# Kernel optimization log

Hardware: AMD Instinct MI355X
Metric: run time of the kernel (lower is better)

Reference implementation:

```python
import jax, jax.numpy as jnp
import numpy as np

B = 4096
INPUT = 1024
HIDDEN = 2048
D_INNER = 2 * HIDDEN      # expand=2
DT_RANK = HIDDEN // 16    # 128
D_STATE = 16
LN_EPS = 1e-5


def setup_inputs() -> dict:
    key = jax.random.key(0)
    ks = jax.random.split(key, 12)
    s = lambda fan_in: 1.0 / np.sqrt(fan_in)
    inp = {
        "x": jax.random.normal(ks[0], (B, INPUT), jnp.float32),
        "h": jax.random.normal(ks[1], (B, HIDDEN), jnp.float32),
        # in_proj: Linear(input_size, 2*d_inner, bias=False)
        "W_in": jax.random.uniform(ks[2], (2 * D_INNER, INPUT), jnp.float32, -s(INPUT), s(INPUT)),
        # state_proj: Linear(hidden, d_inner, bias=False)
        "W_state": jax.random.uniform(ks[3], (D_INNER, HIDDEN), jnp.float32, -s(HIDDEN), s(HIDDEN)),
        # x_proj: Linear(d_inner, dt_rank + 2*d_state, bias=False)
        "W_xproj": jax.random.uniform(ks[4], (DT_RANK + 2 * D_STATE, D_INNER), jnp.float32, -s(D_INNER), s(D_INNER)),
        # dt_proj: Linear(dt_rank, d_inner, bias=True), weight ~ U(-dt_rank^-0.5, dt_rank^-0.5)
        "W_dt": jax.random.uniform(ks[5], (D_INNER, DT_RANK), jnp.float32, -s(DT_RANK), s(DT_RANK)),
        "b_dt": jnp.log(jnp.expm1(jnp.exp(jax.random.uniform(ks[6], (D_INNER,), jnp.float32)
                                           * (np.log(0.1) - np.log(0.001)) + np.log(0.001)))),
        # A_log = log(arange(1, d_state+1)) repeated over d_inner (unused in single-step math)
        "A_log": jnp.broadcast_to(jnp.log(jnp.arange(1, D_STATE + 1, dtype=jnp.float32)), (D_INNER, D_STATE)),
        "D": jnp.ones((D_INNER,), jnp.float32),
        # out_proj: Linear(d_inner, hidden, bias=False)
        "W_out": jax.random.uniform(ks[7], (HIDDEN, D_INNER), jnp.float32, -s(D_INNER), s(D_INNER)),
        # LayerNorm(hidden)
        "gamma": jnp.ones((HIDDEN,), jnp.float32),
        "beta": jnp.zeros((HIDDEN,), jnp.float32),
    }
    return inp


def _layernorm(x, gamma, beta):
    mu = jnp.mean(x, axis=-1, keepdims=True)
    var = jnp.mean(jnp.square(x - mu), axis=-1, keepdims=True)
    return (x - mu) * jax.lax.rsqrt(var + LN_EPS) * gamma + beta


def reference(x, h, W_in, W_state, W_xproj, W_dt, b_dt, A_log, D, W_out, gamma, beta):
    # in_proj and split into x branch / gate z
    xz = x @ W_in.T                               # [B, 2*d_inner]
    x_br, z = jnp.split(xz, 2, axis=-1)
    # add projected previous hidden state, then SiLU
    x_br = jax.nn.silu(x_br + h @ W_state.T)      # [B, d_inner]
    # x_proj -> (dt, B_mat, C)
    x_dbl = x_br @ W_xproj.T                      # [B, dt_rank + 2*d_state]
    dt_lo = x_dbl[:, :DT_RANK]
    B_mat = x_dbl[:, DT_RANK:DT_RANK + D_STATE]   # [B, d_state]
    C_mat = x_dbl[:, DT_RANK + D_STATE:]          # [B, d_state]
    dt = jax.nn.softplus(dt_lo @ W_dt.T + b_dt)   # [B, d_inner]
    # ssm_out[b,d] = sum_n dt[b,d]*B[b,n]*x_br[b,d]*C[b,n] + D[d]*x_br[b,d]
    bc = jnp.sum(B_mat * C_mat, axis=-1, keepdims=True)  # [B, 1]
    ssm_out = dt * x_br * bc + D * x_br           # [B, d_inner]
    # gate, output projection, residual, layernorm
    y = ssm_out * jax.nn.silu(z)
    h_new = y @ W_out.T + h
    return _layernorm(h_new, gamma, beta)
```

## Files before the change

### kernel.cpp

```cpp
#include <hip/hip_runtime.h>
#include <hip/hip_bf16.h>
#include <cstdint>
#include <cstddef>

typedef unsigned short u16;
typedef __bf16 bf16x8 __attribute__((ext_vector_type(8)));
typedef float f32x4 __attribute__((ext_vector_type(4)));

#define B_ROWS 4096
#define N_HIDDEN 2048
#define DT_RANK 128

static __device__ __forceinline__ u16 f2bf(float f) {
  unsigned u = __float_as_uint(f);
  u += 0x7FFFu + ((u >> 16) & 1u);
  return (u16)(u >> 16);
}
static __device__ __forceinline__ float bf2f(u16 b) {
  return __uint_as_float(((unsigned)b) << 16);
}
static __device__ __forceinline__ float siluf(float v) {
  return v / (1.0f + __expf(-v));
}
static __device__ __forceinline__ float softplusf(float v) {
  return v > 15.0f ? v : log1pf(__expf(v));
}
static __device__ __forceinline__ void async16(void* lds, const void* g) {
  __builtin_amdgcn_global_load_lds((const __attribute__((address_space(1))) void*)g,
                                   (__attribute__((address_space(3))) void*)lds, 16, 0, 0);
}

struct CvtJobs {
  const float* src[8];
  u16* dst[8];
  int rl4[8];
  int dstride[8];
  int cum[9];
};
__global__ __launch_bounds__(256)
void cvt_all_kernel(CvtJobs J) {
  int b = blockIdx.x;
  int job = 0;
#pragma unroll
  for (int k = 1; k < 8; ++k) if (b >= J.cum[k]) job = k;
  const int row = b - J.cum[job];
  const int rl4 = J.rl4[job];
  const float4* s = (const float4*)(J.src[job] + (size_t)row * (rl4 * 4));
  ushort4* d = (ushort4*)(J.dst[job] + (size_t)row * J.dstride[job]);
  for (int c = threadIdx.x; c < rl4; c += blockDim.x) {
    float4 f = s[c];
    ushort4 o;
    o.x = f2bf(f.x); o.y = f2bf(f.y); o.z = f2bf(f.z); o.w = f2bf(f.w);
    d[c] = o;
  }
}

template <int NN, int KK, int LDA, int LDB, int EPI, int GX, int GY, int RH, int RW>
__global__ __launch_bounds__(512, 1)
void gemm8(const u16* __restrict__ A, const u16* __restrict__ Bw,
           float* __restrict__ outf, u16* __restrict__ outb, long long zstride)
{
  extern __shared__ u16 lds[];
  u16* ldsA = lds;
  u16* ldsB = lds + 32768;
  constexpr int NT = KK / 64;
  static_assert(NT >= 2, "schedule assumes NT >= 2");
  static_assert(GX * GY == 8 * RH * RW, "rect must partition grid over 8 XCDs");
  static_assert(GX % RW == 0 && GY % RH == 0, "rect divides grid");
  constexpr int XCOLS = GX / RW;
  static_assert((GY / RH) * XCOLS == 8, "XCD grid must be 8");

  const int t = threadIdx.x;
  const int lane = t & 63, w = t >> 6;
  const int wr = w >> 2, wc = w & 3;
  const int r = lane & 15;
  const int q4 = lane >> 4;

  const int bid = blockIdx.y * GX + blockIdx.x;
  const int xcd = bid & 7;
  const int i = bid >> 3;
  const int xr = xcd / XCOLS, xc = xcd % XCOLS;
  const int m0 = (xr * RH + i / RW) * 256;
  const int n0 = (xc * RW + i % RW) * 256;
  const int koff = blockIdx.z * KK;

  f32x4 acc[2][2][4][2] = {};

  auto stA = [&](int buf, int half, int k0) {
#pragma unroll
    for (int i2 = 0; i2 < 2; ++i2) {
      const int ii = w * 2 + i2;
      const int c = ii * 64 + lane;
      const int row = c >> 3;
      const int ch = (c & 7) ^ (row & 7);
      async16(ldsA + (buf * 2 + half) * 8192 + ii * 512,
              A + (size_t)(m0 + half * 128 + row) * LDA + (koff + k0 + ch * 8));
    }
  };
  auto stB = [&](int buf, int half, int k0) {
#pragma unroll
    for (int i2 = 0; i2 < 2; ++i2) {
      const int ii = w * 2 + i2;
      const int c = ii * 64 + lane;
      const int row = c >> 3;
      const int ch = (c & 7) ^ (row & 7);
      async16(ldsB + (buf * 2 + half) * 8192 + ii * 512,
              Bw + (size_t)(n0 + half * 128 + row) * LDB + (koff + k0 + ch * 8));
    }
  };

  auto ldA = [&](int buf, int half, int lr, int kki) -> bf16x8 {
    const int tt = kki * 4 + q4;
    return *(const bf16x8*)(ldsA + (size_t)((buf * 2 + half) * 8192 + lr * 64 + ((tt ^ (lr & 7)) << 3)));
  };
  auto ldB = [&](int buf, int half, int lr, int kki) -> bf16x8 {
    const int tt = kki * 4 + q4;
    return *(const bf16x8*)(ldsB + (size_t)((buf * 2 + half) * 8192 + lr * 64 + ((tt ^ (lr & 7)) << 3)));
  };

  stA(0, 0, 0); stB(0, 0, 0); stB(0, 1, 0); stA(0, 1, 0);
  asm volatile("s_waitcnt vmcnt(4)" ::: "memory");
  __builtin_amdgcn_s_barrier();
  asm volatile("" ::: "memory");

  int cur = 0;
  for (int j = 0; j < NT; ++j) {
    const int nxt = cur ^ 1;
    const bool lastj = (j == NT - 1);
    bf16x8 fa[8], fah[8], fb0[4], fb1[4];

#pragma unroll
    for (int fi = 0; fi < 4; ++fi)
#pragma unroll
      for (int ks = 0; ks < 2; ++ks)
        fa[fi * 2 + ks] = ldA(cur, 0, wr * 64 + fi * 16 + r, ks);
#pragma unroll
    for (int g = 0; g < 2; ++g)
#pragma unroll
      for (int ks = 0; ks < 2; ++ks)
        fb0[g * 2 + ks] = ldB(cur, 0, wc * 32 + g * 16 + r, ks);
    if (j + 1 < NT) stA(nxt, 0, (j + 1) * 64);
    asm volatile("" ::: "memory");
    __builtin_amdgcn_s_barrier();
    asm volatile("s_waitcnt lgkmcnt(0)" ::: "memory");
    __builtin_amdgcn_s_setprio(1);
#pragma unroll
    for (int fi = 0; fi < 4; ++fi)
#pragma unroll
      for (int g = 0; g < 2; ++g) {
        acc[0][0][fi][g] = __builtin_amdgcn_mfma_f32_16x16x32_bf16(fa[fi * 2 + 0], fb0[g * 2 + 0], acc[0][0][fi][g], 0, 0, 0);
        acc[0][0][fi][g] = __builtin_amdgcn_mfma_f32_16x16x32_bf16(fa[fi * 2 + 1], fb0[g * 2 + 1], acc[0][0][fi][g], 0, 0, 0);
      }
    __builtin_amdgcn_s_setprio(0);
    if (lastj) { asm volatile("s_waitcnt vmcnt(2)" ::: "memory"); }
    else       { asm volatile("s_waitcnt vmcnt(4)" ::: "memory"); }
    __builtin_amdgcn_s_barrier();
    asm volatile("" ::: "memory");

#pragma unroll
    for (int g = 0; g < 2; ++g)
#pragma unroll
      for (int ks = 0; ks < 2; ++ks)
        fb1[g * 2 + ks] = ldB(cur, 1, wc * 32 + g * 16 + r, ks);
    if (j + 1 < NT) stB(nxt, 0, (j + 1) * 64);
    asm volatile("" ::: "memory");
    __builtin_amdgcn_s_barrier();
    asm volatile("s_waitcnt lgkmcnt(0)" ::: "memory");
    __builtin_amdgcn_s_setprio(1);
#pragma unroll
    for (int fi = 0; fi < 4; ++fi)
#pragma unroll
      for (int g = 0; g < 2; ++g) {
        acc[0][1][fi][g] = __builtin_amdgcn_mfma_f32_16x16x32_bf16(fa[fi * 2 + 0], fb1[g * 2 + 0], acc[0][1][fi][g], 0, 0, 0);
        acc[0][1][fi][g] = __builtin_amdgcn_mfma_f32_16x16x32_bf16(fa[fi * 2 + 1], fb1[g * 2 + 1], acc[0][1][fi][g], 0, 0, 0);
      }
    __builtin_amdgcn_s_setprio(0);
    if (lastj) { asm volatile("s_waitcnt vmcnt(0)" ::: "memory"); }
    else       { asm volatile("s_waitcnt vmcnt(4)" ::: "memory"); }
    __builtin_amdgcn_s_barrier();
    asm volatile("" ::: "memory");

#pragma unroll
    for (int fi = 0; fi < 4; ++fi)
#pragma unroll
      for (int ks = 0; ks < 2; ++ks)
        fah[fi * 2 + ks] = ldA(cur, 1, wr * 64 + fi * 16 + r, ks);
    if (j + 1 < NT) stB(nxt, 1, (j + 1) * 64);
    asm volatile("" ::: "memory");
    __builtin_amdgcn_s_barrier();
    asm volatile("s_waitcnt lgkmcnt(0)" ::: "memory");
    __builtin_amdgcn_s_setprio(1);
#pragma unroll
    for (int fi = 0; fi < 4; ++fi)
#pragma unroll
      for (int g = 0; g < 2; ++g) {
        acc[1][0][fi][g] = __builtin_amdgcn_mfma_f32_16x16x32_bf16(fah[fi * 2 + 0], fb0[g * 2 + 0], acc[1][0][fi][g], 0, 0, 0);
        acc[1][0][fi][g] = __builtin_amdgcn_mfma_f32_16x16x32_bf16(fah[fi * 2 + 1], fb0[g * 2 + 1], acc[1][0][fi][g], 0, 0, 0);
      }
    __builtin_amdgcn_s_setprio(0);
    asm volatile("" ::: "memory");
    __builtin_amdgcn_s_barrier();
    asm volatile("" ::: "memory");

    if (j + 1 < NT) stA(nxt, 1, (j + 1) * 64);
    asm volatile("" ::: "memory");
    __builtin_amdgcn_s_barrier();
    __builtin_amdgcn_s_setprio(1);
#pragma unroll
    for (int fi = 0; fi < 4; ++fi)
#pragma unroll
      for (int g = 0; g < 2; ++g) {
        acc[1][1][fi][g] = __builtin_amdgcn_mfma_f32_16x16x32_bf16(fah[fi * 2 + 0], fb1[g * 2 + 0], acc[1][1][fi][g], 0, 0, 0);
        acc[1][1][fi][g] = __builtin_amdgcn_mfma_f32_16x16x32_bf16(fah[fi * 2 + 1], fb1[g * 2 + 1], acc[1][1][fi][g], 0, 0, 0);
      }
    __builtin_amdgcn_s_setprio(0);
    if (j + 1 < NT) { asm volatile("s_waitcnt vmcnt(4)" ::: "memory"); }
    asm volatile("" ::: "memory");
    __builtin_amdgcn_s_barrier();
    asm volatile("" ::: "memory");
    cur = nxt;
  }

  float* of = outf ? (outf + (size_t)blockIdx.z * zstride) : nullptr;
#pragma unroll
  for (int a = 0; a < 2; ++a)
#pragma unroll
    for (int b = 0; b < 2; ++b)
#pragma unroll
      for (int fi = 0; fi < 4; ++fi)
#pragma unroll
        for (int g = 0; g < 2; ++g)
#pragma unroll
          for (int tt = 0; tt < 4; ++tt) {
            const int grow = m0 + a * 128 + wr * 64 + fi * 16 + q4 * 4 + tt;
            const int gcol = n0 + b * 128 + wc * 32 + g * 16 + r;
            const float v = acc[a][b][fi][g][tt];
            if constexpr (EPI == 0) {
              outb[(size_t)grow * NN + gcol] = f2bf(siluf(v));
            } else {
              of[(size_t)grow * NN + gcol] = v;
            }
          }
}

template <int NN, int KK, int LDA, int EPI>
__global__ __launch_bounds__(256)
void gemm_bt(const u16* __restrict__ A, const u16* __restrict__ Bw,
             float* __restrict__ outf, u16* __restrict__ outb,
             const float* __restrict__ aux1, const float* __restrict__ aux2,
             const float* __restrict__ aux3,
             const u16* __restrict__ xaux, const u16* __restrict__ saux)
{
  constexpr int BM = 128, BK = 64;
  __shared__ alignas(16) u16 As[2][BM * BK];
  __shared__ alignas(16) u16 Bs[2][BM * BK];
  const int t = threadIdx.x;
  const int lane = t & 63, w = t >> 6;
  const int m0 = blockIdx.y * BM, n0 = blockIdx.x * BM;
  const int mw = (w >> 1) * 64, nw = (w & 1) * 64;
  const int r = lane & 15;
  const int kq = (lane >> 4) * 8;

  f32x4 acc[4][4] = {};

  auto stage = [&](int buf, int k0) {
#pragma unroll
    for (int i = 0; i < 4; ++i) {
      const int slot0 = (w * 4 + i) * 64;
      const int s = slot0 + lane;
      const int row = s >> 3, cs = (s & 7) * 8;
      async16(&As[buf][slot0 * 8], A + (size_t)(m0 + row) * LDA + k0 + cs);
      async16(&Bs[buf][slot0 * 8], Bw + (size_t)(n0 + row) * KK + k0 + cs);
    }
  };

  stage(0, 0);
  asm volatile("s_waitcnt vmcnt(0)" ::: "memory");
  __syncthreads();
  int cur = 0;

  for (int k0 = 0; k0 < KK; k0 += BK) {
    if (k0 + BK < KK) stage(cur ^ 1, k0 + BK);
#pragma unroll
    for (int kk = 0; kk < BK; kk += 32) {
      bf16x8 af[4], bb[4];
#pragma unroll
      for (int f = 0; f < 4; ++f)
        af[f] = *(const bf16x8*)(&As[cur][(mw + f * 16 + r) * BK + kk + kq]);
#pragma unroll
      for (int f = 0; f < 4; ++f)
        bb[f] = *(const bf16x8*)(&Bs[cur][(nw + f * 16 + r) * BK + kk + kq]);
#pragma unroll
      for (int fm = 0; fm < 4; ++fm)
#pragma unroll
        for (int fn = 0; fn < 4; ++fn)
          acc[fm][fn] = __builtin_amdgcn_mfma_f32_16x16x32_bf16(af[fm], bb[fn], acc[fm][fn], 0, 0, 0);
    }
    asm volatile("s_waitcnt vmcnt(0)" ::: "memory");
    __syncthreads();
    cur ^= 1;
  }

  const int rr = (lane >> 4) * 4;
  const int cc = lane & 15;
#pragma unroll
  for (int fm = 0; fm < 4; ++fm) {
#pragma unroll
    for (int fn = 0; fn < 4; ++fn) {
#pragma unroll
      for (int tt = 0; tt < 4; ++tt) {
        const int grow = m0 + mw + fm * 16 + rr + tt;
        const int gcol = n0 + nw + fn * 16 + cc;
        float v = acc[fm][fn][tt];
        if constexpr (EPI == 2) {
          float dt = softplusf(v + aux1[gcol]);
          float xv = bf2f(xaux[(size_t)grow * NN + gcol]);
          float sv = bf2f(saux[(size_t)grow * NN + gcol]);
          float yv = xv * (dt * aux2[grow] + aux3[gcol]) * sv;
          outb[(size_t)grow * NN + gcol] = f2bf(yv);
        } else {
          outf[(size_t)grow * NN + gcol] = v;
        }
      }
    }
  }
}

__global__ __launch_bounds__(256)
void gemm_xproj(const u16* __restrict__ A, const u16* __restrict__ Bw,
                float* __restrict__ part)
{
  constexpr int BK = 64;
  __shared__ alignas(16) u16 As[64 * BK];
  __shared__ alignas(16) u16 Bs[160 * BK];
  const int t = threadIdx.x, lane = t & 63, w = t >> 6;
  const int m0 = blockIdx.x * 64;
  const int kz = blockIdx.y;
  const int r = lane & 15, kq = (lane >> 4) * 8;
  f32x4 acc[10] = {};
  for (int kt = 0; kt < 1024; kt += BK) {
    const int k0 = kz * 1024 + kt;
#pragma unroll
    for (int i = 0; i < 2; ++i) {
      const int slot0 = (w * 2 + i) * 64;
      const int s = slot0 + lane;
      async16(As + slot0 * 8, A + (size_t)(m0 + (s >> 3)) * 4096 + k0 + (s & 7) * 8);
    }
#pragma unroll
    for (int i = 0; i < 5; ++i) {
      const int slot0 = (w * 5 + i) * 64;
      const int s = slot0 + lane;
      async16(Bs + slot0 * 8, Bw + (size_t)(s >> 3) * 4096 + k0 + (s & 7) * 8);
    }
    asm volatile("s_waitcnt vmcnt(0)" ::: "memory");
    __syncthreads();
#pragma unroll
    for (int kk = 0; kk < BK; kk += 32) {
      bf16x8 af = *(const bf16x8*)(As + (w * 16 + r) * BK + kk + kq);
#pragma unroll
      for (int fn = 0; fn < 10; ++fn) {
        bf16x8 bb = *(const bf16x8*)(Bs + (fn * 16 + r) * BK + kk + kq);
        acc[fn] = __builtin_amdgcn_mfma_f32_16x16x32_bf16(af, bb, acc[fn], 0, 0, 0);
      }
    }
    __syncthreads();
  }
  float* o = part + (size_t)kz * B_ROWS * 160;
  const int rr = (lane >> 4) * 4, cc = lane & 15;
#pragma unroll
  for (int fn = 0; fn < 10; ++fn)
#pragma unroll
    for (int tt = 0; tt < 4; ++tt)
      o[(size_t)(m0 + w * 16 + rr + tt) * 160 + fn * 16 + cc] = acc[fn][tt];
}

__global__ __launch_bounds__(192)
void xdbl_reduce(const float* __restrict__ part, u16* __restrict__ dtlo,
                 float* __restrict__ bc)
{
  const int row = blockIdx.x, t = threadIdx.x;
  __shared__ float cvals[32];
  float v = 0.0f;
  if (t < 160) {
    const float* p = part + (size_t)row * 160 + t;
#pragma unroll
    for (int z = 0; z < 4; ++z) v += p[(size_t)z * B_ROWS * 160];
  }
  if (t < DT_RANK) dtlo[(size_t)row * DT_RANK + t] = f2bf(v);
  if (t >= DT_RANK && t < 160) cvals[t - DT_RANK] = v;
  __syncthreads();
  if (t == 0) {
    float s = 0.0f;
#pragma unroll
    for (int j = 0; j < 16; ++j) s += cvals[j] * cvals[j + 16];
    bc[row] = s;
  }
}

__global__ __launch_bounds__(256)
void ln_kernel(const float* __restrict__ p0, const float* __restrict__ p1,
               const float* __restrict__ hh, const float* __restrict__ gamma,
               const float* __restrict__ beta, float* __restrict__ out)
{
  const int row = blockIdx.x, t = threadIdx.x;
  __shared__ float red[4];
  const float4* x0 = (const float4*)(p0 + (size_t)row * N_HIDDEN);
  const float4* x1 = (const float4*)(p1 + (size_t)row * N_HIDDEN);
  const float4* xh = (const float4*)(hh + (size_t)row * N_HIDDEN);
  float4 a, b;
  {
    float4 u = x0[t], v = x1[t], w = xh[t];
    a.x = u.x + v.x + w.x; a.y = u.y + v.y + w.y; a.z = u.z + v.z + w.z; a.w = u.w + v.w + w.w;
    u = x0[t + 256]; v = x1[t + 256]; w = xh[t + 256];
    b.x = u.x + v.x + w.x; b.y = u.y + v.y + w.y; b.z = u.z + v.z + w.z; b.w = u.w + v.w + w.w;
  }
  float s = ((a.x + a.y) + (a.z + a.w)) + ((b.x + b.y) + (b.z + b.w));
#pragma unroll
  for (int m = 32; m; m >>= 1) s += __shfl_xor(s, m);
  if ((t & 63) == 0) red[t >> 6] = s;
  __syncthreads();
  s = (red[0] + red[1]) + (red[2] + red[3]);
  const float mu = s * (1.0f / N_HIDDEN);
  float dx0 = a.x - mu, dx1 = a.y - mu, dx2 = a.z - mu, dx3 = a.w - mu;
  float dy0 = b.x - mu, dy1 = b.y - mu, dy2 = b.z - mu, dy3 = b.w - mu;
  float q = ((dx0 * dx0 + dx1 * dx1) + (dx2 * dx2 + dx3 * dx3)) +
            ((dy0 * dy0 + dy1 * dy1) + (dy2 * dy2 + dy3 * dy3));
  __syncthreads();
#pragma unroll
  for (int m = 32; m; m >>= 1) q += __shfl_xor(q, m);
  if ((t & 63) == 0) red[t >> 6] = q;
  __syncthreads();
  q = (red[0] + red[1]) + (red[2] + red[3]);
  const float inv = rsqrtf(q * (1.0f / N_HIDDEN) + 1e-5f);
  const float4 ga = ((const float4*)gamma)[t], gb = ((const float4*)gamma)[t + 256];
  const float4 ba = ((const float4*)beta)[t], bbv = ((const float4*)beta)[t + 256];
  float4 o0, o1;
  o0.x = dx0 * inv * ga.x + ba.x;
  o0.y = dx1 * inv * ga.y + ba.y;
  o0.z = dx2 * inv * ga.z + ba.z;
  o0.w = dx3 * inv * ga.w + ba.w;
  o1.x = dy0 * inv * gb.x + bbv.x;
  o1.y = dy1 * inv * gb.y + bbv.y;
  o1.z = dy2 * inv * gb.z + bbv.z;
  o1.w = dy3 * inv * gb.w + bbv.w;
  float4* o4 = (float4*)(out + (size_t)row * N_HIDDEN);
  o4[t] = o0;
  o4[t + 256] = o1;
}

extern "C" void kernel_launch(void* const* d_in, const int* in_sizes, int n_in,
                              void* d_out, int out_size, void* d_ws, size_t ws_size,
                              hipStream_t stream) {
  const float* x     = (const float*)d_in[0];
  const float* h     = (const float*)d_in[1];
  const float* W_in  = (const float*)d_in[2];
  const float* W_st  = (const float*)d_in[3];
  const float* W_xp  = (const float*)d_in[4];
  const float* W_dt  = (const float*)d_in[5];
  const float* b_dt  = (const float*)d_in[6];
  const float* Dv    = (const float*)d_in[8];
  const float* W_out = (const float*)d_in[9];
  const float* gamma = (const float*)d_in[10];
  const float* beta  = (const float*)d_in[11];
  float* out = (float*)d_out;
  (void)in_sizes; (void)n_in; (void)out_size; (void)ws_size;

  char* ws = (char*)d_ws;
  size_t o = 0;
  auto alloc = [&](size_t bytes) { char* p = ws + o; o += bytes; return p; };
  u16* Acat    = (u16*)alloc((size_t)4096 * 3072 * 2);
  u16* Wcat    = (u16*)alloc((size_t)4096 * 3072 * 2);
  u16* Wz_bf   = (u16*)alloc((size_t)4096 * 1024 * 2);
  u16* Wxp_bf  = (u16*)alloc((size_t)160 * 4096 * 2);
  u16* Wdt_bf  = (u16*)alloc((size_t)4096 * 128 * 2);
  u16* Wout_bf = (u16*)alloc((size_t)2048 * 4096 * 2);
  u16* xbr_bf  = (u16*)alloc((size_t)4096 * 4096 * 2);
  u16* sz_bf   = (u16*)alloc((size_t)4096 * 4096 * 2);
  float* part  = (float*)alloc((size_t)4 * 4096 * 160 * 4);
  u16* dtlo_bf = (u16*)alloc((size_t)4096 * 128 * 2);
  float* bc    = (float*)alloc((size_t)4096 * 4);
  u16* y_bf = (u16*)Acat;
  float* p0 = (float*)xbr_bf;
  float* p1 = p0 + (size_t)4096 * 2048;

  CvtJobs J;
  J.src[0] = x;                           J.dst[0] = Acat;        J.rl4[0] = 256;  J.dstride[0] = 3072;
  J.src[1] = h;                           J.dst[1] = Acat + 1024; J.rl4[1] = 512;  J.dstride[1] = 3072;
  J.src[2] = W_in;                        J.dst[2] = Wcat;        J.rl4[2] = 256;  J.dstride[2] = 3072;
  J.src[3] = W_st;                        J.dst[3] = Wcat + 1024; J.rl4[3] = 512;  J.dstride[3] = 3072;
  J.src[4] = W_in + (size_t)4096 * 1024;  J.dst[4] = Wz_bf;       J.rl4[4] = 256;  J.dstride[4] = 1024;
  J.src[5] = W_xp;                        J.dst[5] = Wxp_bf;      J.rl4[5] = 1024; J.dstride[5] = 4096;
  J.src[6] = W_dt;                        J.dst[6] = Wdt_bf;      J.rl4[6] = 32;   J.dstride[6] = 128;
  J.src[7] = W_out;                       J.dst[7] = Wout_bf;     J.rl4[7] = 1024; J.dstride[7] = 4096;
  const int rows[8] = {4096, 4096, 4096, 4096, 4096, 160, 4096, 2048};
  J.cum[0] = 0;
  for (int k = 0; k < 8; ++k) J.cum[k + 1] = J.cum[k] + rows[k];
  cvt_all_kernel<<<J.cum[8], 256, 0, stream>>>(J);

  gemm8<4096, 3072, 3072, 3072, 0, 16, 16, 4, 8><<<dim3(16, 16, 1), 512, 131072, stream>>>(
      Acat, Wcat, nullptr, xbr_bf, 0);
  gemm8<4096, 1024, 3072, 1024, 0, 16, 16, 4, 8><<<dim3(16, 16, 1), 512, 131072, stream>>>(
      Acat, Wz_bf, nullptr, sz_bf, 0);
  gemm_xproj<<<dim3(64, 4), 256, 0, stream>>>(xbr_bf, Wxp_bf, part);
  xdbl_reduce<<<4096, 192, 0, stream>>>(part, dtlo_bf, bc);
  gemm_bt<4096, 128, 128, 2><<<dim3(32, 32), 256, 0, stream>>>(
      dtlo_bf, Wdt_bf, nullptr, y_bf, b_dt, bc, Dv, xbr_bf, sz_bf);
  gemm8<2048, 2048, 4096, 4096, 1, 8, 16, 4, 4><<<dim3(8, 16, 2), 512, 131072, stream>>>(
      y_bf, Wout_bf, p0, nullptr, (long long)4096 * 2048);
  ln_kernel<<<4096, 256, 0, stream>>>(p0, p1, h, gamma, beta, out);
}
```

Measured before the change: 358.4 us.

## Deepen GEMM prefetch to stage loads two K-tiles ahead with unrolled buffers

Restructures the bf16 MFMA GEMM main loop so global-to-LDS async loads are issued up to two K-steps ahead rather than one, with a deeper prologue and loosened vmcnt waits. The loop is unrolled by two so buffer indices become compile-time constants, and the swizzled LDS read addresses are precomputed once. The aim is to hide more global memory latency and cut address arithmetic. It requires an even K-tile count of at least 4, and the reordered waits carry a risk of races if the vmcnt accounting is wrong.

```diff
diff --git a/kernel.cpp b/kernel.cpp
--- a/kernel.cpp
+++ b/kernel.cpp
@@ -64,7 +64,7 @@
   u16* ldsA = lds;
   u16* ldsB = lds + 32768;
   constexpr int NT = KK / 64;
-  static_assert(NT >= 2, "schedule assumes NT >= 2");
+  static_assert(NT >= 4 && (NT % 2) == 0, "schedule assumes even NT >= 4");
   static_assert(GX * GY == 8 * RH * RW, "rect must partition grid over 8 XCDs");
   static_assert(GX % RW == 0 && GY % RH == 0, "rect divides grid");
   constexpr int XCOLS = GX / RW;
@@ -109,116 +109,118 @@
     }
   };
 
-  auto ldA = [&](int buf, int half, int lr, int kki) -> bf16x8 {
-    const int tt = kki * 4 + q4;
-    return *(const bf16x8*)(ldsA + (size_t)((buf * 2 + half) * 8192 + lr * 64 + ((tt ^ (lr & 7)) << 3)));
-  };
-  auto ldB = [&](int buf, int half, int lr, int kki) -> bf16x8 {
-    const int tt = kki * 4 + q4;
-    return *(const bf16x8*)(ldsB + (size_t)((buf * 2 + half) * 8192 + lr * 64 + ((tt ^ (lr & 7)) << 3)));
-  };
+  const int rb = r & 7;
+  const int s0 = (q4 ^ rb) << 3;
+  const int s1 = ((4 + q4) ^ rb) << 3;
+  const u16* baA0 = ldsA + (wr * 64 + r) * 64 + s0;
+  const u16* baA1 = ldsA + (wr * 64 + r) * 64 + s1;
+  const u16* baB0 = ldsB + (wc * 32 + r) * 64 + s0;
+  const u16* baB1 = ldsB + (wc * 32 + r) * 64 + s1;
 
   stA(0, 0, 0); stB(0, 0, 0); stB(0, 1, 0); stA(0, 1, 0);
-  asm volatile("s_waitcnt vmcnt(4)" ::: "memory");
+  stA(1, 0, 64); stB(1, 0, 64); stB(1, 1, 64);
+  asm volatile("s_waitcnt vmcnt(6)" ::: "memory");
   __builtin_amdgcn_s_barrier();
   asm volatile("" ::: "memory");
 
-  int cur = 0;
-  for (int j = 0; j < NT; ++j) {
-    const int nxt = cur ^ 1;
-    const bool lastj = (j == NT - 1);
-    bf16x8 fa[8], fah[8], fb0[4], fb1[4];
-
-#pragma unroll
-    for (int fi = 0; fi < 4; ++fi)
-#pragma unroll
-      for (int ks = 0; ks < 2; ++ks)
-        fa[fi * 2 + ks] = ldA(cur, 0, wr * 64 + fi * 16 + r, ks);
-#pragma unroll
-    for (int g = 0; g < 2; ++g)
-#pragma unroll
-      for (int ks = 0; ks < 2; ++ks)
-        fb0[g * 2 + ks] = ldB(cur, 0, wc * 32 + g * 16 + r, ks);
-    if (j + 1 < NT) stA(nxt, 0, (j + 1) * 64);
-    asm volatile("" ::: "memory");
-    __builtin_amdgcn_s_barrier();
-    asm volatile("s_waitcnt lgkmcnt(0)" ::: "memory");
-    __builtin_amdgcn_s_setprio(1);
-#pragma unroll
-    for (int fi = 0; fi < 4; ++fi)
+  for (int j0 = 0; j0 < NT; j0 += 2) {
+#pragma unroll
+    for (int u = 0; u < 2; ++u) {
+      const int j = j0 + u;
+      constexpr int SL = 8192;
+      const int CB = u * 2 * SL;
+      const int NB = (u ^ 1) * 2 * SL;
+      bf16x8 fa[8], fah[8], fb0v[4], fb1v[4];
+
+#pragma unroll
+      for (int fi = 0; fi < 4; ++fi) {
+        fa[fi * 2 + 0] = *(const bf16x8*)(baA0 + CB + fi * 1024);
+        fa[fi * 2 + 1] = *(const bf16x8*)(baA1 + CB + fi * 1024);
+      }
 #pragma unroll
       for (int g = 0; g < 2; ++g) {
-        acc[0][0][fi][g] = __builtin_amdgcn_mfma_f32_16x16x32_bf16(fa[fi * 2 + 0], fb0[g * 2 + 0], acc[0][0][fi][g], 0, 0, 0);
-        acc[0][0][fi][g] = __builtin_amdgcn_mfma_f32_16x16x32_bf16(fa[fi * 2 + 1], fb0[g * 2 + 1], acc[0][0][fi][g], 0, 0, 0);
+        fb0v[g * 2 + 0] = *(const bf16x8*)(baB0 + CB + g * 1024);
+        fb0v[g * 2 + 1] = *(const bf16x8*)(baB1 + CB + g * 1024);
       }
-    __builtin_amdgcn_s_setprio(0);
-    if (lastj) { asm volatile("s_waitcnt vmcnt(2)" ::: "memory"); }
-    else       { asm volatile("s_waitcnt vmcnt(4)" ::: "memory"); }
-    __builtin_amdgcn_s_barrier();
-    asm volatile("" ::: "memory");
-
-#pragma unroll
-    for (int g = 0; g < 2; ++g)
-#pragma unroll
-      for (int ks = 0; ks < 2; ++ks)
-        fb1[g * 2 + ks] = ldB(cur, 1, wc * 32 + g * 16 + r, ks);
-    if (j + 1 < NT) stB(nxt, 0, (j + 1) * 64);
-    asm volatile("" ::: "memory");
-    __builtin_amdgcn_s_barrier();
-    asm volatile("s_waitcnt lgkmcnt(0)" ::: "memory");
-    __builtin_amdgcn_s_setprio(1);
-#pragma unroll
-    for (int fi = 0; fi < 4; ++fi)
+      if (j + 1 < NT) stA(u ^ 1, 1, (j + 1) * 64);
+      asm volatile("" ::: "memory");
+      __builtin_amdgcn_s_barrier();
+      asm volatile("s_waitcnt lgkmcnt(0)" ::: "memory");
+      __builtin_amdgcn_s_setprio(1);
+#pragma unroll
+      for (int fi = 0; fi < 4; ++fi)
+#pragma unroll
+        for (int g = 0; g < 2; ++g) {
+          acc[0][0][fi][g] = __builtin_amdgcn_mfma_f32_16x16x32_bf16(fa[fi * 2 + 0], fb0v[g * 2 + 0], acc[0][0][fi][g], 0, 0, 0);
+          acc[0][0][fi][g] = __builtin_amdgcn_mfma_f32_16x16x32_bf16(fa[fi * 2 + 1], fb0v[g * 2 + 1], acc[0][0][fi][g], 0, 0, 0);
+        }
+      __builtin_amdgcn_s_setprio(0);
+      asm volatile("" ::: "memory");
+      __builtin_amdgcn_s_barrier();
+      asm volatile("" ::: "memory");
+
 #pragma unroll
       for (int g = 0; g < 2; ++g) {
-        acc[0][1][fi][g] = __builtin_amdgcn_mfma_f32_16x16x32_bf16(fa[fi * 2 + 0], fb1[g * 2 + 0], acc[0][1][fi][g], 0, 0, 0);
-        acc[0][1][fi][g] = __builtin_amdgcn_mfma_f32_16x16x32_bf16(fa[fi * 2 + 1], fb1[g * 2 + 1], acc[0][1][fi][g], 0, 0, 0);
+        fb1v[g * 2 + 0] = *(const bf16x8*)(baB0 + CB + SL + g * 1024);
+        fb1v[g * 2 + 1] = *(const bf16x8*)(baB1 + CB + SL + g * 1024);
       }
-    __builtin_amdgcn_s_setprio(0);
-    if (lastj) { asm volatile("s_waitcnt vmcnt(0)" ::: "memory"); }
-    else       { asm volatile("s_waitcnt vmcnt(4)" ::: "memory"); }
-    __builtin_amdgcn_s_barrier();
-    asm volatile("" ::: "memory");
-
-#pragma unroll
-    for (int fi = 0; fi < 4; ++fi)
-#pragma unroll
-      for (int ks = 0; ks < 2; ++ks)
-        fah[fi * 2 + ks] = ldA(cur, 1, wr * 64 + fi * 16 + r, ks);
-    if (j + 1 < NT) stB(nxt, 1, (j + 1) * 64);
-    asm volatile("" ::: "memory");
-    __builtin_amdgcn_s_barrier();
-    asm volatile("s_waitcnt lgkmcnt(0)" ::: "memory");
-    __builtin_amdgcn_s_setprio(1);
-#pragma unroll
-    for (int fi = 0; fi < 4; ++fi)
-#pragma unroll
-      for (int g = 0; g < 2; ++g) {
-        acc[1][0][fi][g] = __builtin_amdgcn_mfma_f32_16x16x32_bf16(fah[fi * 2 + 0], fb0[g * 2 + 0], acc[1][0][fi][g], 0, 0, 0);
-        acc[1][0][fi][g] = __builtin_amdgcn_mfma_f32_16x16x32_bf16(fah[fi * 2 + 1], fb0[g * 2 + 1], acc[1][0][fi][g], 0, 0, 0);
+      if (j + 2 < NT) stA(u, 0, (j + 2) * 64);
+      asm volatile("" ::: "memory");
+      __builtin_amdgcn_s_barrier();
+      asm volatile("s_waitcnt lgkmcnt(0)" ::: "memory");
+      __builtin_amdgcn_s_setprio(1);
+#pragma unroll
+      for (int fi = 0; fi < 4; ++fi)
+#pragma unroll
+        for (int g = 0; g < 2; ++g) {
+          acc[0][1][fi][g] = __builtin_amdgcn_mfma_f32_16x16x32_bf16(fa[fi * 2 + 0], fb1v[g * 2 + 0], acc[0][1][fi][g], 0, 0, 0);
+          acc[0][1][fi][g] = __builtin_amdgcn_mfma_f32_16x16x32_bf16(fa[fi * 2 + 1], fb1v[g * 2 + 1], acc[0][1][fi][g], 0, 0, 0);
+        }
+      __builtin_amdgcn_s_setprio(0);
+      asm volatile("" ::: "memory");
+      __builtin_amdgcn_s_barrier();
+      asm volatile("" ::: "memory");
+
+#pragma unroll
+      for (int fi = 0; fi < 4; ++fi) {
+        fah[fi * 2 + 0] = *(const bf16x8*)(baA0 + CB + SL + fi * 1024);
+        fah[fi * 2 + 1] = *(const bf16x8*)(baA1 + CB + SL + fi * 1024);
       }
-    __builtin_amdgcn_s_setprio(0);
-    asm volatile("" ::: "memory");
-    __builtin_amdgcn_s_barrier();
-    asm volatile("" ::: "memory");
-
-    if (j + 1 < NT) stA(nxt, 1, (j + 1) * 64);
-    asm volatile("" ::: "memory");
-    __builtin_amdgcn_s_barrier();
-    __builtin_amdgcn_s_setprio(1);
-#pragma unroll
-    for (int fi = 0; fi < 4; ++fi)
-#pragma unroll
-      for (int g = 0; g < 2; ++g) {
-        acc[1][1][fi][g] = __builtin_amdgcn_mfma_f32_16x16x32_bf16(fah[fi * 2 + 0], fb1[g * 2 + 0], acc[1][1][fi][g], 0, 0, 0);
-        acc[1][1][fi][g] = __builtin_amdgcn_mfma_f32_16x16x32_bf16(fah[fi * 2 + 1], fb1[g * 2 + 1], acc[1][1][fi][g], 0, 0, 0);
-      }
-    __builtin_amdgcn_s_setprio(0);
-    if (j + 1 < NT) { asm volatile("s_waitcnt vmcnt(4)" ::: "memory"); }
-    asm volatile("" ::: "memory");
-    __builtin_amdgcn_s_barrier();
-    asm volatile("" ::: "memory");
-    cur = nxt;
+      if (j + 2 < NT) stB(u, 0, (j + 2) * 64);
+      asm volatile("" ::: "memory");
+      __builtin_amdgcn_s_barrier();
+      asm volatile("s_waitcnt lgkmcnt(0)" ::: "memory");
+      __builtin_amdgcn_s_setprio(1);
+#pragma unroll
+      for (int fi = 0; fi < 4; ++fi)
+#pragma unroll
+        for (int g = 0; g < 2; ++g) {
+          acc[1][0][fi][g] = __builtin_amdgcn_mfma_f32_16x16x32_bf16(fah[fi * 2 + 0], fb0v[g * 2 + 0], acc[1][0][fi][g], 0, 0, 0);
+          acc[1][0][fi][g] = __builtin_amdgcn_mfma_f32_16x16x32_bf16(fah[fi * 2 + 1], fb0v[g * 2 + 1], acc[1][0][fi][g], 0, 0, 0);
+        }
+      __builtin_amdgcn_s_setprio(0);
+      asm volatile("" ::: "memory");
+      __builtin_amdgcn_s_barrier();
+      asm volatile("" ::: "memory");
+
+      if (j + 2 < NT) stB(u, 1, (j + 2) * 64);
+      asm volatile("" ::: "memory");
+      __builtin_amdgcn_s_barrier();
+      __builtin_amdgcn_s_setprio(1);
+#pragma unroll
+      for (int fi = 0; fi < 4; ++fi)
+#pragma unroll
+        for (int g = 0; g < 2; ++g) {
+          acc[1][1][fi][g] = __builtin_amdgcn_mfma_f32_16x16x32_bf16(fah[fi * 2 + 0], fb1v[g * 2 + 0], acc[1][1][fi][g], 0, 0, 0);
+          acc[1][1][fi][g] = __builtin_amdgcn_mfma_f32_16x16x32_bf16(fah[fi * 2 + 1], fb1v[g * 2 + 1], acc[1][1][fi][g], 0, 0, 0);
+        }
+      __builtin_amdgcn_s_setprio(0);
+      if (j + 2 < NT)      { asm volatile("s_waitcnt vmcnt(6)" ::: "memory"); }
+      else if (j + 1 < NT) { asm volatile("s_waitcnt vmcnt(0)" ::: "memory"); }
+      asm volatile("" ::: "memory");
+      __builtin_amdgcn_s_barrier();
+      asm volatile("" ::: "memory");
+    }
   }
 
   float* of = outf ? (outf + (size_t)blockIdx.z * zstride) : nullptr;
```

Measured after the change: 363.8 us. No clear change (+1.5%).
